# Optimization experiments

Hardware: AMD Instinct MI355X
Metric: run time of the kernel (lower is better)

## Reference

```python
import jax, jax.numpy as jnp
import numpy as np


def _jacobian_circulant(v):
    """Spatial Jacobian of a 3D vector field with circulant boundaries.

    v : (B, X, Y, Z, D) velocity field (channels last)
    returns J : (B, X, Y, Z, D, D) with J[..., i, j] = d v_i / d x_j,
    computed by central differences with wrap-around (circulant) bounds.
    """
    cols = []
    for j in range(3):
        ax = 1 + j  # spatial axis for coordinate j
        g = (jnp.roll(v, -1, axis=ax) - jnp.roll(v, 1, axis=ax)) * 0.5
        cols.append(g)
    return jnp.stack(cols, axis=-1)  # (B, X, Y, Z, D, D)


def _bracket(x, y):
    """Lie bracket of two velocity fields: [x, y] = J_x y - J_y x."""
    jx = _jacobian_circulant(x)
    jy = _jacobian_circulant(y)
    return (jnp.einsum('bxyzij,bxyzj->bxyzi', jx, y)
            - jnp.einsum('bxyzij,bxyzj->bxyzi', jy, x))


def _bch(x, y, trunc=2):
    """Truncated BCH series: z s.t. exp(z) = exp(x) o exp(y)."""
    z = x + y
    if trunc >= 2:
        z = z + 0.5 * _bracket(x, y)
    return z


def setup_inputs() -> dict:
    key = jax.random.key(0)
    k1, k2 = jax.random.split(key)
    B, D, X, Y, Z = 2, 3, 128, 128, 128
    left = jax.random.normal(k1, (B, D, X, Y, Z), dtype=jnp.float32)
    right = jax.random.normal(k2, (B, D, X, Y, Z), dtype=jnp.float32)
    return {"left": left, "right": right}


def reference(left, right):
    # (B, D, *shape) -> channels-last (B, *shape, D)
    l = jnp.moveaxis(left, 1, -1)
    r = jnp.moveaxis(right, 1, -1)
    v = _bch(l, r, trunc=2)
    return jnp.moveaxis(v, -1, 1)
```

## Files before the change

### kernel.cpp

```cpp
#include <hip/hip_runtime.h>


namespace {
constexpr int Xd = 128, Yd = 128, Zd = 128, Dd = 3;
constexpr int Sd  = Xd * Yd * Zd;
constexpr int YZd = Yd * Zd;
constexpr int YT  = 8;
constexpr int NXCD = 8;

typedef float f32x4_t __attribute__((ext_vector_type(4)));

__device__ inline float4 f4sub(float4 a, float4 b) {
    return make_float4(a.x - b.x, a.y - b.y, a.z - b.z, a.w - b.w);
}
__device__ inline float4 f4add(float4 a, float4 b) {
    return make_float4(a.x + b.x, a.y + b.y, a.z + b.z, a.w + b.w);
}
__device__ inline float4 f4mul(float4 a, float4 b) {
    return make_float4(a.x * b.x, a.y * b.y, a.z * b.z, a.w * b.w);
}
__device__ inline float4 f4fma(float4 a, float4 b, float4 c) {
    return make_float4(fmaf(a.x, b.x, c.x), fmaf(a.y, b.y, c.y),
                       fmaf(a.z, b.z, c.z), fmaf(a.w, b.w, c.w));
}
__device__ inline float4 f4fms(float4 a, float4 b, float4 c) {
    return make_float4(fmaf(-a.x, b.x, c.x), fmaf(-a.y, b.y, c.y),
                       fmaf(-a.z, b.z, c.z), fmaf(-a.w, b.w, c.w));
}
__device__ inline void store_nt(float* p, float4 v) {
    __builtin_nontemporal_store(*(const f32x4_t*)&v, (f32x4_t*)p);
}
}

__global__ void __launch_bounds__(256)
bch_gather(const float* __restrict__ L, const float* __restrict__ R,
           float* __restrict__ O)
{
    const int t  = threadIdx.x;
    const int zc = t & 31;
    const int ly = t >> 5;

    const int bid = blockIdx.x;
    int bb = (bid & (NXCD - 1)) * (4096 / NXCD) + (bid >> 3);

    const int yt = bb & 15; bb >>= 4;
    const int x  = bb & 127; bb >>= 7;
    const int b  = bb;

    const int y  = yt * YT + ly;
    const int z0 = zc * 4;

    const int fbase = b * (Dd * Sd) + x * YZd + y * Zd + z0;
    const float* pL = L + fbase;
    const float* pR = R + fbase;
    float*       pO = O + fbase;

    const int oxp = (((x + 1) & 127) - x) * YZd;
    const int oxm = (((x - 1) & 127) - x) * YZd;
    const int oym = (((y - 1) & 127) - y) * Zd;
    const int oyp = (((y + 1) & 127) - y) * Zd;
    const int zlm = (zc + 31) & 31;
    const int zlp = (zc + 1) & 31;

    float4 BL[3], BR[3];
    float4 XPL[3], XML[3], XPR[3], XMR[3];
    float4 YPL[3], YML[3], YPR[3], YMR[3];
#pragma unroll
    for (int d = 0; d < 3; ++d) {
        BL[d]  = *(const float4*)(pL + d * Sd);
        BR[d]  = *(const float4*)(pR + d * Sd);
        XPL[d] = *(const float4*)(pL + oxp + d * Sd);
        XML[d] = *(const float4*)(pL + oxm + d * Sd);
        XPR[d] = *(const float4*)(pR + oxp + d * Sd);
        XMR[d] = *(const float4*)(pR + oxm + d * Sd);
        YPL[d] = *(const float4*)(pL + oyp + d * Sd);
        YML[d] = *(const float4*)(pL + oym + d * Sd);
        YPR[d] = *(const float4*)(pR + oyp + d * Sd);
        YMR[d] = *(const float4*)(pR + oym + d * Sd);
    }

#pragma unroll
    for (int i = 0; i < 3; ++i) {
        float4 dl = f4sub(XPL[i], XML[i]);
        float4 dr = f4sub(XPR[i], XMR[i]);
        float4 br = f4fms(dr, BL[0], f4mul(dl, BR[0]));

        dl = f4sub(YPL[i], YML[i]);
        dr = f4sub(YPR[i], YMR[i]);
        br = f4fms(dr, BL[1], f4fma(dl, BR[1], br));

        const float lzm = __shfl(BL[i].w, zlm, 32);
        const float lzp = __shfl(BL[i].x, zlp, 32);
        const float rzm = __shfl(BR[i].w, zlm, 32);
        const float rzp = __shfl(BR[i].x, zlp, 32);
        dl = make_float4(BL[i].y - lzm, BL[i].z - BL[i].x,
                         BL[i].w - BL[i].y, lzp - BL[i].z);
        dr = make_float4(BR[i].y - rzm, BR[i].z - BR[i].x,
                         BR[i].w - BR[i].y, rzp - BR[i].z);
        br = f4fms(dr, BL[2], f4fma(dl, BR[2], br));

        float4 out = f4add(BL[i], BR[i]);
        const float4 q = make_float4(0.25f, 0.25f, 0.25f, 0.25f);
        out = f4fma(q, br, out);
        store_nt(pO + i * Sd, out);
    }
}

extern "C" void kernel_launch(void* const* d_in, const int* in_sizes, int n_in,
                              void* d_out, int out_size, void* d_ws, size_t ws_size,
                              hipStream_t stream)
{
    const float* L = (const float*)d_in[0];
    const float* R = (const float*)d_in[1];
    float*       O = (float*)d_out;

    const int nblocks = (Yd / YT) * Xd * 2;
    bch_gather<<<dim3(nblocks), dim3(256), 0, stream>>>(L, R, O);
}
```

Measured before the change: 144.1 us.

## Process two x-planes per thread to reuse loaded x-neighbors in registers

Each block now covers a pair of adjacent x-planes instead of one. The center values of one plane serve as the x-neighbors of the other, which cuts global loads per output from 10 to 8 float4 per channel pair. The cost is higher register pressure and half as many blocks, which may lower occupancy and reduce latency hiding.

```diff
diff --git a/kernel.cpp b/kernel.cpp
--- a/kernel.cpp
+++ b/kernel.cpp
@@ -7,6 +7,7 @@
 constexpr int YZd = Yd * Zd;
 constexpr int YT  = 8;
 constexpr int NXCD = 8;
+constexpr int NBLK = (Yd / YT) * (Xd / 2) * 2;
 
 typedef float f32x4_t __attribute__((ext_vector_type(4)));
 
@@ -33,77 +34,98 @@
 }
 
 __global__ void __launch_bounds__(256)
-bch_gather(const float* __restrict__ L, const float* __restrict__ R,
-           float* __restrict__ O)
+bch_pair(const float* __restrict__ L, const float* __restrict__ R,
+         float* __restrict__ O)
 {
     const int t  = threadIdx.x;
     const int zc = t & 31;
     const int ly = t >> 5;
 
     const int bid = blockIdx.x;
-    int bb = (bid & (NXCD - 1)) * (4096 / NXCD) + (bid >> 3);
+    int bb = (bid & (NXCD - 1)) * (NBLK / NXCD) + (bid >> 3);
 
     const int yt = bb & 15; bb >>= 4;
-    const int x  = bb & 127; bb >>= 7;
+    const int xp = bb & 63; bb >>= 6;
     const int b  = bb;
 
+    const int x0 = xp * 2;
     const int y  = yt * YT + ly;
     const int z0 = zc * 4;
 
-    const int fbase = b * (Dd * Sd) + x * YZd + y * Zd + z0;
+    const int fbase = b * (Dd * Sd) + x0 * YZd + y * Zd + z0;
     const float* pL = L + fbase;
     const float* pR = R + fbase;
     float*       pO = O + fbase;
 
-    const int oxp = (((x + 1) & 127) - x) * YZd;
-    const int oxm = (((x - 1) & 127) - x) * YZd;
+    const int oxm = (((x0 - 1) & 127) - x0) * YZd;
+    const int ox2 = (((x0 + 2) & 127) - x0) * YZd;
     const int oym = (((y - 1) & 127) - y) * Zd;
     const int oyp = (((y + 1) & 127) - y) * Zd;
     const int zlm = (zc + 31) & 31;
     const int zlp = (zc + 1) & 31;
 
-    float4 BL[3], BR[3];
-    float4 XPL[3], XML[3], XPR[3], XMR[3];
-    float4 YPL[3], YML[3], YPR[3], YMR[3];
+    auto compute_store = [&](const float4 (&CL)[3],  const float4 (&CR)[3],
+                             const float4 (&XPL)[3], const float4 (&XPR)[3],
+                             const float4 (&XML)[3], const float4 (&XMR)[3],
+                             const float4 (&YPL)[3], const float4 (&YPR)[3],
+                             const float4 (&YML)[3], const float4 (&YMR)[3],
+                             int ooff) {
+#pragma unroll
+        for (int i = 0; i < 3; ++i) {
+            float4 dl = f4sub(XPL[i], XML[i]);
+            float4 dr = f4sub(XPR[i], XMR[i]);
+            float4 br = f4fms(dr, CL[0], f4mul(dl, CR[0]));
+
+            dl = f4sub(YPL[i], YML[i]);
+            dr = f4sub(YPR[i], YMR[i]);
+            br = f4fms(dr, CL[1], f4fma(dl, CR[1], br));
+
+            const float lzm = __shfl(CL[i].w, zlm, 32);
+            const float lzp = __shfl(CL[i].x, zlp, 32);
+            const float rzm = __shfl(CR[i].w, zlm, 32);
+            const float rzp = __shfl(CR[i].x, zlp, 32);
+            dl = make_float4(CL[i].y - lzm, CL[i].z - CL[i].x,
+                             CL[i].w - CL[i].y, lzp - CL[i].z);
+            dr = make_float4(CR[i].y - rzm, CR[i].z - CR[i].x,
+                             CR[i].w - CR[i].y, rzp - CR[i].z);
+            br = f4fms(dr, CL[2], f4fma(dl, CR[2], br));
+
+            float4 out = f4add(CL[i], CR[i]);
+            const float4 q = make_float4(0.25f, 0.25f, 0.25f, 0.25f);
+            out = f4fma(q, br, out);
+            store_nt(pO + ooff + i * Sd, out);
+        }
+    };
+
+    float4 XmL[3], XmR[3];
+    float4 C0L[3], C0R[3];
+    float4 C1L[3], C1R[3];
+    float4 YpL[3], YmL[3], YpR[3], YmR[3];
 #pragma unroll
     for (int d = 0; d < 3; ++d) {
-        BL[d]  = *(const float4*)(pL + d * Sd);
-        BR[d]  = *(const float4*)(pR + d * Sd);
-        XPL[d] = *(const float4*)(pL + oxp + d * Sd);
-        XML[d] = *(const float4*)(pL + oxm + d * Sd);
-        XPR[d] = *(const float4*)(pR + oxp + d * Sd);
-        XMR[d] = *(const float4*)(pR + oxm + d * Sd);
-        YPL[d] = *(const float4*)(pL + oyp + d * Sd);
-        YML[d] = *(const float4*)(pL + oym + d * Sd);
-        YPR[d] = *(const float4*)(pR + oyp + d * Sd);
-        YMR[d] = *(const float4*)(pR + oym + d * Sd);
+        XmL[d] = *(const float4*)(pL + oxm + d * Sd);
+        XmR[d] = *(const float4*)(pR + oxm + d * Sd);
+        C0L[d] = *(const float4*)(pL + d * Sd);
+        C0R[d] = *(const float4*)(pR + d * Sd);
+        C1L[d] = *(const float4*)(pL + YZd + d * Sd);
+        C1R[d] = *(const float4*)(pR + YZd + d * Sd);
+        YpL[d] = *(const float4*)(pL + oyp + d * Sd);
+        YmL[d] = *(const float4*)(pL + oym + d * Sd);
+        YpR[d] = *(const float4*)(pR + oyp + d * Sd);
+        YmR[d] = *(const float4*)(pR + oym + d * Sd);
     }
+    compute_store(C0L, C0R, C1L, C1R, XmL, XmR, YpL, YpR, YmL, YmR, 0);
 
 #pragma unroll
-    for (int i = 0; i < 3; ++i) {
-        float4 dl = f4sub(XPL[i], XML[i]);
-        float4 dr = f4sub(XPR[i], XMR[i]);
-        float4 br = f4fms(dr, BL[0], f4mul(dl, BR[0]));
-
-        dl = f4sub(YPL[i], YML[i]);
-        dr = f4sub(YPR[i], YMR[i]);
-        br = f4fms(dr, BL[1], f4fma(dl, BR[1], br));
-
-        const float lzm = __shfl(BL[i].w, zlm, 32);
-        const float lzp = __shfl(BL[i].x, zlp, 32);
-        const float rzm = __shfl(BR[i].w, zlm, 32);
-        const float rzp = __shfl(BR[i].x, zlp, 32);
-        dl = make_float4(BL[i].y - lzm, BL[i].z - BL[i].x,
-                         BL[i].w - BL[i].y, lzp - BL[i].z);
-        dr = make_float4(BR[i].y - rzm, BR[i].z - BR[i].x,
-                         BR[i].w - BR[i].y, rzp - BR[i].z);
-        br = f4fms(dr, BL[2], f4fma(dl, BR[2], br));
-
-        float4 out = f4add(BL[i], BR[i]);
-        const float4 q = make_float4(0.25f, 0.25f, 0.25f, 0.25f);
-        out = f4fma(q, br, out);
-        store_nt(pO + i * Sd, out);
+    for (int d = 0; d < 3; ++d) {
+        XmL[d] = *(const float4*)(pL + ox2 + d * Sd);
+        XmR[d] = *(const float4*)(pR + ox2 + d * Sd);
+        YpL[d] = *(const float4*)(pL + YZd + oyp + d * Sd);
+        YmL[d] = *(const float4*)(pL + YZd + oym + d * Sd);
+        YpR[d] = *(const float4*)(pR + YZd + oyp + d * Sd);
+        YmR[d] = *(const float4*)(pR + YZd + oym + d * Sd);
     }
+    compute_store(C1L, C1R, XmL, XmR, C0L, C0R, YpL, YpR, YmL, YmR, YZd);
 }
 
 extern "C" void kernel_launch(void* const* d_in, const int* in_sizes, int n_in,
@@ -114,6 +136,5 @@
     const float* R = (const float*)d_in[1];
     float*       O = (float*)d_out;
 
-    const int nblocks = (Yd / YT) * Xd * 2;
-    bch_gather<<<dim3(nblocks), dim3(256), 0, stream>>>(L, R, O);
+    bch_pair<<<dim3(NBLK), dim3(256), 0, stream>>>(L, R, O);
 }
```

Measured after the change: 144.0 us. No clear change (-0.1%).
